# Optimization experiments

Hardware: AMD Instinct MI355X
Metric: run time of the kernel (lower is better)

Reference implementation:

```python
import jax, jax.numpy as jnp
import numpy as np

N_MICS = 8
MIC_RADIUS = 0.05
SAMPLE_RATE = 16000.0
SPEED_SOUND = 343.0
EPS = 1e-20
SPHERE_LEVELS = 4


def sphere_np(levels=SPHERE_LEVELS):
    # Faithful numpy port of the torch icosphere subdivision in sphere().
    h = 5.0 ** 0.5 / 5.0
    r = 2.0 / 5.0 * 5.0 ** 0.5
    pi = 3.141592654
    pts = np.zeros((12, 3), dtype=np.float32)
    pts[0] = [0.0, 0.0, 1.0]
    pts[11] = [0.0, 0.0, -1.0]
    k = np.arange(5, dtype=np.float32)
    pts[1:6, 0] = r * np.sin(2.0 * pi * k / 5.0)
    pts[1:6, 1] = r * np.cos(2.0 * pi * k / 5.0)
    pts[1:6, 2] = h
    pts[6:11, 0] = -r * np.sin(2.0 * pi * k / 5.0)
    pts[6:11, 1] = -r * np.cos(2.0 * pi * k / 5.0)
    pts[6:11, 2] = -h
    trs = np.array([[0, 2, 1], [0, 3, 2], [0, 4, 3], [0, 5, 4], [0, 1, 5],
                    [9, 1, 2], [10, 2, 3], [6, 3, 4], [7, 4, 5], [8, 5, 1],
                    [4, 7, 6], [5, 8, 7], [1, 9, 8], [2, 10, 9], [3, 6, 10],
                    [11, 6, 7], [11, 7, 8], [11, 8, 9], [11, 9, 10], [11, 10, 6]], dtype=np.int64)
    for _ in range(levels):
        T = trs.shape[0]
        sub = np.zeros((4 * T, 6), dtype=np.int64)
        sub[0 * T:1 * T] = trs[:, [0, 0, 0, 1, 2, 0]]
        sub[1 * T:2 * T] = trs[:, [0, 1, 1, 1, 1, 2]]
        sub[2 * T:3 * T] = trs[:, [2, 0, 1, 2, 2, 2]]
        sub[3 * T:4 * T] = trs[:, [0, 1, 1, 2, 2, 0]]
        flat = np.concatenate((sub[:, [0, 1]], sub[:, [2, 3]], sub[:, [4, 5]]), axis=0)
        srt = np.sort(flat, axis=1)
        m = srt.max()
        scal = srt[:, 0] * (m + 1) + srt[:, 1]
        uniq, inv = np.unique(scal, return_inverse=True)
        uv0 = uniq // (m + 1)
        uv1 = uniq - uv0 * (m + 1)
        trs = inv.reshape(3, -1).T
        pts = pts[uv0] + pts[uv1]
        pts /= np.sqrt((pts ** 2).sum(axis=1, keepdims=True))
    return pts.astype(np.float32)


def setup_inputs() -> dict:
    key = jax.random.key(0)
    # DOA grid and TDOAs from array geometry (precomputed in SrpPhat.__init__)
    doas_np = sphere_np()                                    # [2562, 3]
    ang = 2.0 * np.pi * np.arange(N_MICS) / N_MICS
    mics_np = np.stack([MIC_RADIUS * np.cos(ang), MIC_RADIUS * np.sin(ang),
                        np.zeros(N_MICS)], axis=1).astype(np.float32)  # [8, 3]
    taus_np = (SAMPLE_RATE / SPEED_SOUND) * (doas_np @ mics_np.T)      # [2562, 8]
    B, T, F, P = 4, 250, 513, N_MICS * (N_MICS + 1) // 2
    XXs = jax.random.normal(key, (B, T, F, 2, P), dtype=jnp.float32)
    return {"XXs": XXs, "taus": jnp.asarray(taus_np), "doas": jnp.asarray(doas_np)}


def reference(XXs, taus, doas):
    B, T, F, _, P = XXs.shape
    n_mics = taus.shape[1]
    D = taus.shape[0]
    frame_size = (F - 1) * 2
    # Steering phases: a = exp(-j * omega * tau)   [D, F, M]
    omegas = 2.0 * jnp.pi * jnp.arange(F, dtype=jnp.float32) / frame_size
    phase = omegas[None, :, None] * taus[:, None, :]
    A_re = jnp.cos(phase)
    A_im = -jnp.sin(phase)
    # Cross steering terms for every mic pair (triu incl. diagonal): W = a_i * conj(a_j)^H form
    i0, i1 = np.triu_indices(n_mics)                         # 36 pairs for 8 mics
    Ws_re = A_re[:, :, i0] * A_re[:, :, i1] + A_im[:, :, i0] * A_im[:, :, i1]  # [D, F, P]
    Ws_im = A_re[:, :, i0] * A_im[:, :, i1] - A_im[:, :, i0] * A_re[:, :, i1]
    # PHAT normalization of the cross-spectra
    XX_re = XXs[:, :, :, 0, :]
    XX_im = XXs[:, :, :, 1, :]
    mag = jnp.sqrt(XX_re ** 2 + XX_im ** 2) + EPS
    Xr = (XX_re / mag).reshape(B, T, F * P)
    Xi = (XX_im / mag).reshape(B, T, F * P)
    Wr = Ws_re.reshape(D, F * P)
    Wi = Ws_im.reshape(D, F * P)
    # SRP map: Re{ sum_fp XX_norm * conj(W) } reduced over freqs and pairs
    Ys = jnp.matmul(Xr, Wr.T) + jnp.matmul(Xi, Wi.T)         # [B, T, D]
    idx = jnp.argmax(Ys, axis=2)                             # [B, T]
    return doas[idx]                                         # [B, T, 3]
```

## Files before the change

kernel.cpp:

```cpp
#include <hip/hip_runtime.h>
#include <math.h>


#define F_BINS  513
#define M_TOTAL 1000
#define D_TOTAL 2562
#define D_PAD   2688
#define NPAIR   28
#define NC      32
#define K2      (NPAIR * NC)
#define S_SCALE 4.67f
#define NBT     4
#define CNT     8
#define FSPLIT  12
#define KSPB    4
#define KPS     224
#define BT_PAD  1024

#define OFF_COEF 0
#define OFF_TT   16512
#define OFF_GT   (OFF_TT + (size_t)K2 * D_PAD)
#define OFF_GP   (OFF_GT + (size_t)K2 * BT_PAD)
#define OFF_YS   OFF_GP

__device__ __constant__ int c_ptab[NPAIR] = {1,2,3,4,5,6,7, 9,10,11,12,13,14,
                                             16,17,18,19,20, 22,23,24,25,
                                             27,28,29, 31,32, 34};
__device__ __constant__ int c_i0[NPAIR] = {0,0,0,0,0,0,0, 1,1,1,1,1,1,
                                           2,2,2,2,2, 3,3,3,3, 4,4,4, 5,5, 6};
__device__ __constant__ int c_i1[NPAIR] = {1,2,3,4,5,6,7, 2,3,4,5,6,7,
                                           3,4,5,6,7, 4,5,6,7, 5,6,7, 6,7, 7};
__device__ __constant__ int c_inv[36] = {
    -1, 0, 1, 2, 3, 4, 5, 6,
    -1, 7, 8, 9,10,11,12,
    -1,13,14,15,16,17,
    -1,18,19,20,21,
    -1,22,23,24,
    -1,25,26,
    -1,27,
    -1};

__global__ void k_coef(float* __restrict__ coefEO) {
    __shared__ double sHC[NC][NC + 1];
    __shared__ double sHS[NC][NC + 1];
    const int f = blockIdx.x;
    const int t = threadIdx.x;
    const double z = (double)f * (M_PI / 512.0) * (double)S_SCALE;
    double th = M_PI * (t + 0.5) / NC;
    double ct = cos(th);
    double hs, hc;
    sincos(z * ct, &hs, &hc);
    double cp = 1.0, cc = ct, c2 = 2.0 * ct;
    sHC[0][t] = hc;      sHS[0][t] = hs;
    sHC[1][t] = hc * cc; sHS[1][t] = hs * cc;
    for (int n = 2; n < NC; ++n) {
        double cn = c2 * cc - cp;
        cp = cc; cc = cn;
        sHC[n][t] = hc * cn;
        sHS[n][t] = hs * cn;
    }
    __syncthreads();
    const int n = (t < 16) ? 2 * t : 2 * (t - 16) + 1;
    double sum = 0.0;
    if (t < 16) { for (int j = 0; j < NC; ++j) sum += sHC[n][j]; }
    else        { for (int j = 0; j < NC; ++j) sum += sHS[n][j]; }
    double scale = (n == 0) ? (1.0 / NC) : (2.0 / NC);
    coefEO[f * 32 + t] = (float)(sum * scale);
}

__global__ void k_ttab(const float* __restrict__ taus, float* __restrict__ Tt) {
    const int d = blockIdx.x * 256 + threadIdx.x;
    const int p = blockIdx.y;
    if (d >= D_PAD) return;
    const bool live = d < D_TOTAL;
    const int dd = live ? d : 0;
    const float u = (taus[dd * 8 + c_i0[p]] - taus[dd * 8 + c_i1[p]]) * (1.0f / S_SCALE);
    float* base = Tt + (size_t)p * 32 * D_PAD + d;
    base[0] = live ? 1.f : 0.f;
    base[(size_t)16 * D_PAD] = live ? u : 0.f;
    float tp = 1.f, tc = u;
    const float u2 = 2.f * u;
    for (int n = 2; n < NC; ++n) {
        float tn = u2 * tc - tp;
        tp = tc; tc = tn;
        int c = (n & 1) ? 16 + (n >> 1) : (n >> 1);
        base[(size_t)c * D_PAD] = live ? tn : 0.f;
    }
}

#define NSLOT 3
__global__ __launch_bounds__(128, 3) void k_stageA(
    const float* __restrict__ XXs, const float* __restrict__ coefEO,
    float* __restrict__ Gp)
{
    __shared__ float4 sXn4[NBT][CNT / 4][64];
    __shared__ float  sCall[48][32];
    const int t     = threadIdx.x;
    const int bt0   = blockIdx.x * NBT;
    const int split = blockIdx.y;
    const int fbeg  = (F_BINS * split) / FSPLIT;
    const int fend  = (F_BINS * (split + 1)) / FSPLIT;
    const int p   = t & 31;
    const int sel = t >> 5;
    const bool im = sel >= 2;
    const int row = (p < NPAIR ? p : NPAIR - 1) + (im ? 32 : 0);
    const int c0  = (sel & 1) * 8 + (im ? 16 : 0);

    for (int e = t; e < 48 * 8; e += 128) {
        int fl = e >> 3, q = e & 7;
        int f  = fbeg + fl; if (f > F_BINS - 1) f = F_BINS - 1;
        *(float4*)&sCall[fl][q * 4] = *(const float4*)&coefEO[f * 32 + q * 4];
    }

    const float* srcs[NSLOT];
    float*       dstb[NSLOT];
    int          offj[NSLOT][4];
    int          flv [NSLOT];
    #pragma unroll
    for (int s = 0; s < NSLOT; ++s) {
        int e    = t + s * 128;
        bool act = e < NBT * CNT * 9;
        int ec  = act ? e : 0;
        int q   = ec % 9;
        int rbf = ec / 9;
        int bt  = rbf / CNT;
        int fl  = rbf - bt * CNT;
        flv[s]  = act ? fl : 127;
        srcs[s] = XXs + (((size_t)(bt0 + bt) * F_BINS) + fl) * 72 + q * 4;
        dstb[s] = (float*)&sXn4[bt][fl >> 2][0] + (fl & 3);
        #pragma unroll
        for (int j = 0; j < 4; ++j) {
            int pp = c_inv[q * 4 + j];
            offj[s][j] = (act && pp >= 0) ? pp * 4 : -1;
        }
    }

    float acc[NBT][8] = {};
    float4 cur_re[NSLOT], cur_im[NSLOT], nxt_re[NSLOT], nxt_im[NSLOT];

    auto issue = [&](int fc, float4* vre, float4* vim) {
        const int cnt = fend - fc;
        #pragma unroll
        for (int s = 0; s < NSLOT; ++s) {
            float4 z4 = {0.f, 0.f, 0.f, 0.f};
            vre[s] = z4; vim[s] = z4;
            if (flv[s] < cnt) {
                const float* bp = srcs[s] + (size_t)fc * 72;
                vre[s] = *(const float4*)bp;
                vim[s] = *(const float4*)(bp + 36);
            }
        }
    };

    issue(fbeg, cur_re, cur_im);

    for (int fc = fbeg; fc < fend; fc += CNT) {
        __syncthreads();
        #pragma unroll
        for (int s = 0; s < NSLOT; ++s) {
            const float* xr4 = (const float*)&cur_re[s];
            const float* xi4 = (const float*)&cur_im[s];
            #pragma unroll
            for (int j = 0; j < 4; ++j) {
                int o = offj[s][j];
                if (o >= 0) {
                    float xr = xr4[j], xi = xi4[j];
                    float inv = rsqrtf(xr * xr + xi * xi + 1e-37f);
                    dstb[s][o]       = xr * inv;
                    dstb[s][o + 128] = xi * inv;
                }
            }
        }
        if (fc + CNT < fend) issue(fc + CNT, nxt_re, nxt_im);
        __syncthreads();
        const int cbase = fc - fbeg;
        #pragma unroll
        for (int fg = 0; fg < CNT / 4; ++fg) {
            float4 cjA[4], cjB[4];
            #pragma unroll
            for (int j = 0; j < 4; ++j) {
                cjA[j] = *(const float4*)&sCall[cbase + fg * 4 + j][c0];
                cjB[j] = *(const float4*)&sCall[cbase + fg * 4 + j][c0 + 4];
            }
            #pragma unroll
            for (int bt = 0; bt < NBT; ++bt) {
                float4 a4 = sXn4[bt][fg][row];
                float av[4] = {a4.x, a4.y, a4.z, a4.w};
                #pragma unroll
                for (int j = 0; j < 4; ++j) {
                    acc[bt][0] = fmaf(av[j], cjA[j].x, acc[bt][0]);
                    acc[bt][1] = fmaf(av[j], cjA[j].y, acc[bt][1]);
                    acc[bt][2] = fmaf(av[j], cjA[j].z, acc[bt][2]);
                    acc[bt][3] = fmaf(av[j], cjA[j].w, acc[bt][3]);
                    acc[bt][4] = fmaf(av[j], cjB[j].x, acc[bt][4]);
                    acc[bt][5] = fmaf(av[j], cjB[j].y, acc[bt][5]);
                    acc[bt][6] = fmaf(av[j], cjB[j].z, acc[bt][6]);
                    acc[bt][7] = fmaf(av[j], cjB[j].w, acc[bt][7]);
                }
            }
        }
        #pragma unroll
        for (int s = 0; s < NSLOT; ++s) { cur_re[s] = nxt_re[s]; cur_im[s] = nxt_im[s]; }
    }

    if (p < NPAIR) {
        float* gsp = Gp + (size_t)split * M_TOTAL * K2;
        #pragma unroll
        for (int bt = 0; bt < NBT; ++bt) {
            float* g = gsp + (size_t)(bt0 + bt) * K2 + p * 32 + c0;
            float4 v0 = {acc[bt][0], acc[bt][1], acc[bt][2], acc[bt][3]};
            float4 v1 = {acc[bt][4], acc[bt][5], acc[bt][6], acc[bt][7]};
            *(float4*)&g[0] = v0;
            *(float4*)&g[4] = v1;
        }
    }
}

__global__ __launch_bounds__(256) void k_reduceG(
    const float* __restrict__ Gp, float* __restrict__ Gt)
{
    __shared__ float sT[32][65];
    const int t   = threadIdx.x;
    const int k0  = blockIdx.x * 32;
    const int bt0 = blockIdx.y * 64;
    const size_t MK = (size_t)M_TOTAL * K2;
    #pragma unroll
    for (int i = 0; i < 8; ++i) {
        int e  = t + i * 256;
        int kl = e & 31, btl = e >> 5;
        int bt = bt0 + btl;
        float s = 0.f;
        if (bt < M_TOTAL) {
            const float* g = Gp + (size_t)bt * K2 + k0 + kl;
            #pragma unroll
            for (int pl = 0; pl < FSPLIT; ++pl) s += g[pl * MK];
        }
        sT[kl][btl] = s;
    }
    __syncthreads();
    #pragma unroll
    for (int i = 0; i < 8; ++i) {
        int e   = t + i * 256;
        int btl = e & 63, kl = e >> 6;
        Gt[(size_t)(k0 + kl) * BT_PAD + bt0 + btl] = sT[kl][btl];
    }
}

#define BKB 32
__global__ __launch_bounds__(256, 4) void k_gemmB(
    const float* __restrict__ Gt, const float* __restrict__ Tt,
    float* __restrict__ Ysp)
{
    __shared__ float sA[BKB][260];
    __shared__ float sB[BKB][68];
    const int t = threadIdx.x;
    const int row0 = blockIdx.x * 256;
    const int col0 = blockIdx.y * 64;
    const int koff = blockIdx.z * KPS;
    const int tx = t & 15;
    const int ty = t >> 4;
    float acc[16][4] = {};

    for (int k0 = 0; k0 < KPS; k0 += BKB) {
        __syncthreads();
        #pragma unroll
        for (int i = 0; i < 8; ++i) {
            int e = t + i * 256;
            int kk = e >> 6, r4 = (e & 63) * 4;
            *(float4*)&sA[kk][r4] =
                *(const float4*)&Gt[(size_t)(koff + k0 + kk) * BT_PAD + row0 + r4];
        }
        #pragma unroll
        for (int i = 0; i < 2; ++i) {
            int e = t + i * 256;
            int kk = e >> 4, c4 = (e & 15) * 4;
            *(float4*)&sB[kk][c4] =
                *(const float4*)&Tt[(size_t)(koff + k0 + kk) * D_PAD + col0 + c4];
        }
        __syncthreads();
        #pragma unroll 8
        for (int kk = 0; kk < BKB; ++kk) {
            float4 b  = *(const float4*)&sB[kk][tx * 4];
            float4 a0 = *(const float4*)&sA[kk][ty * 16];
            float4 a1 = *(const float4*)&sA[kk][ty * 16 + 4];
            float4 a2 = *(const float4*)&sA[kk][ty * 16 + 8];
            float4 a3 = *(const float4*)&sA[kk][ty * 16 + 12];
            float av[16] = {a0.x, a0.y, a0.z, a0.w, a1.x, a1.y, a1.z, a1.w,
                            a2.x, a2.y, a2.z, a2.w, a3.x, a3.y, a3.z, a3.w};
            float bv[4] = {b.x, b.y, b.z, b.w};
            #pragma unroll
            for (int i = 0; i < 16; ++i)
                #pragma unroll
                for (int j = 0; j < 4; ++j)
                    acc[i][j] = fmaf(av[i], bv[j], acc[i][j]);
        }
    }
    float* yp = Ysp + (size_t)blockIdx.z * M_TOTAL * D_PAD;
    #pragma unroll
    for (int i = 0; i < 16; ++i) {
        int rg = row0 + ty * 16 + i;
        if (rg >= M_TOTAL) continue;
        float4 v = {acc[i][0], acc[i][1], acc[i][2], acc[i][3]};
        *(float4*)(yp + (size_t)rg * D_PAD + col0 + tx * 4) = v;
    }
}

__global__ __launch_bounds__(256) void k_argmax(
    const float* __restrict__ Ysp, const float* __restrict__ doas,
    float* __restrict__ out)
{
    __shared__ float sv[256];
    __shared__ int   si[256];
    const int row = blockIdx.x;
    const int tid = threadIdx.x;
    const float* y = Ysp + (size_t)row * D_PAD;
    const size_t PL = (size_t)M_TOTAL * D_PAD;
    float best = -INFINITY;
    int bi = D_TOTAL;
    for (int d = tid; d < D_TOTAL; d += 256) {
        float v = y[d] + y[d + PL] + y[d + 2 * PL] + y[d + 3 * PL];
        if (v > best) { best = v; bi = d; }
    }
    sv[tid] = best; si[tid] = bi;
    __syncthreads();
    for (int s = 128; s > 0; s >>= 1) {
        if (tid < s) {
            float v2 = sv[tid + s]; int i2 = si[tid + s];
            if (v2 > sv[tid] || (v2 == sv[tid] && i2 < si[tid])) { sv[tid] = v2; si[tid] = i2; }
        }
        __syncthreads();
    }
    if (tid == 0) {
        int idx = si[0];
        out[row * 3 + 0] = doas[idx * 3 + 0];
        out[row * 3 + 1] = doas[idx * 3 + 1];
        out[row * 3 + 2] = doas[idx * 3 + 2];
    }
}

extern "C" void kernel_launch(void* const* d_in, const int* in_sizes, int n_in,
                              void* d_out, int out_size, void* d_ws, size_t ws_size,
                              hipStream_t stream) {
    const float* XXs  = (const float*)d_in[0];
    const float* taus = (const float*)d_in[1];
    const float* doas = (const float*)d_in[2];
    float* ws     = (float*)d_ws;
    float* coefEO = ws + OFF_COEF;
    float* Tt     = ws + OFF_TT;
    float* Gt     = ws + OFF_GT;
    float* Gp     = ws + OFF_GP;
    float* Ysp    = ws + OFF_YS;

    k_coef   <<<F_BINS, 32, 0, stream>>>(coefEO);
    k_ttab   <<<dim3((D_PAD + 255) / 256, NPAIR), 256, 0, stream>>>(taus, Tt);
    k_stageA <<<dim3(M_TOTAL / NBT, FSPLIT), 128, 0, stream>>>(XXs, coefEO, Gp);
    k_reduceG<<<dim3(K2 / 32, BT_PAD / 64), 256, 0, stream>>>(Gp, Gt);
    k_gemmB  <<<dim3(BT_PAD / 256, D_PAD / 64, KSPB), 256, 0, stream>>>(Gt, Tt, Ysp);
    k_argmax <<<M_TOTAL, 256, 0, stream>>>(Ysp, doas, (float*)d_out);
}
```

Measured before the change: 319.9 us.

## Double-buffer stageA shared tiles and merge coef/ttab init kernels

The stage-A loop now keeps two shared-memory buffers for the normalized cross-spectra and alternates between two register sets. This drops one barrier per chunk and lets the normalize of the next chunk overlap with compute on the current one. The two setup kernels that build the Chebyshev coefficients and the steering table are fused into a single launch, chosen by block index, which saves one kernel launch. In exchange it uses more LDS and registers in stageA, which could lower occupancy, and the coefficient blocks now launch 256 threads of which only 32 do work.

```diff
diff --git a/kernel.cpp b/kernel.cpp
--- a/kernel.cpp
+++ b/kernel.cpp
@@ -16,6 +16,7 @@
 #define KSPB    4
 #define KPS     224
 #define BT_PAD  1024
+#define DBLK    11
 
 #define OFF_COEF 0
 #define OFF_TT   16512
@@ -23,9 +24,6 @@
 #define OFF_GP   (OFF_GT + (size_t)K2 * BT_PAD)
 #define OFF_YS   OFF_GP
 
-__device__ __constant__ int c_ptab[NPAIR] = {1,2,3,4,5,6,7, 9,10,11,12,13,14,
-                                             16,17,18,19,20, 22,23,24,25,
-                                             27,28,29, 31,32, 34};
 __device__ __constant__ int c_i0[NPAIR] = {0,0,0,0,0,0,0, 1,1,1,1,1,1,
                                            2,2,2,2,2, 3,3,3,3, 4,4,4, 5,5, 6};
 __device__ __constant__ int c_i1[NPAIR] = {1,2,3,4,5,6,7, 2,3,4,5,6,7,
@@ -40,51 +38,56 @@
     -1,27,
     -1};
 
-__global__ void k_coef(float* __restrict__ coefEO) {
+__global__ void k_init(const float* __restrict__ taus,
+                       float* __restrict__ coefEO, float* __restrict__ Tt) {
     __shared__ double sHC[NC][NC + 1];
     __shared__ double sHS[NC][NC + 1];
-    const int f = blockIdx.x;
-    const int t = threadIdx.x;
-    const double z = (double)f * (M_PI / 512.0) * (double)S_SCALE;
-    double th = M_PI * (t + 0.5) / NC;
-    double ct = cos(th);
-    double hs, hc;
-    sincos(z * ct, &hs, &hc);
-    double cp = 1.0, cc = ct, c2 = 2.0 * ct;
-    sHC[0][t] = hc;      sHS[0][t] = hs;
-    sHC[1][t] = hc * cc; sHS[1][t] = hs * cc;
-    for (int n = 2; n < NC; ++n) {
-        double cn = c2 * cc - cp;
-        cp = cc; cc = cn;
-        sHC[n][t] = hc * cn;
-        sHS[n][t] = hs * cn;
-    }
-    __syncthreads();
-    const int n = (t < 16) ? 2 * t : 2 * (t - 16) + 1;
-    double sum = 0.0;
-    if (t < 16) { for (int j = 0; j < NC; ++j) sum += sHC[n][j]; }
-    else        { for (int j = 0; j < NC; ++j) sum += sHS[n][j]; }
-    double scale = (n == 0) ? (1.0 / NC) : (2.0 / NC);
-    coefEO[f * 32 + t] = (float)(sum * scale);
-}
-
-__global__ void k_ttab(const float* __restrict__ taus, float* __restrict__ Tt) {
-    const int d = blockIdx.x * 256 + threadIdx.x;
-    const int p = blockIdx.y;
-    if (d >= D_PAD) return;
-    const bool live = d < D_TOTAL;
-    const int dd = live ? d : 0;
-    const float u = (taus[dd * 8 + c_i0[p]] - taus[dd * 8 + c_i1[p]]) * (1.0f / S_SCALE);
-    float* base = Tt + (size_t)p * 32 * D_PAD + d;
-    base[0] = live ? 1.f : 0.f;
-    base[(size_t)16 * D_PAD] = live ? u : 0.f;
-    float tp = 1.f, tc = u;
-    const float u2 = 2.f * u;
-    for (int n = 2; n < NC; ++n) {
-        float tn = u2 * tc - tp;
-        tp = tc; tc = tn;
-        int c = (n & 1) ? 16 + (n >> 1) : (n >> 1);
-        base[(size_t)c * D_PAD] = live ? tn : 0.f;
+    if (blockIdx.x < DBLK * NPAIR) {
+        const int p = blockIdx.x / DBLK;
+        const int d = (blockIdx.x % DBLK) * 256 + threadIdx.x;
+        if (d >= D_PAD) return;
+        const bool live = d < D_TOTAL;
+        const int dd = live ? d : 0;
+        const float u = (taus[dd * 8 + c_i0[p]] - taus[dd * 8 + c_i1[p]]) * (1.0f / S_SCALE);
+        float* base = Tt + (size_t)p * 32 * D_PAD + d;
+        base[0] = live ? 1.f : 0.f;
+        base[(size_t)16 * D_PAD] = live ? u : 0.f;
+        float tp = 1.f, tc = u;
+        const float u2 = 2.f * u;
+        for (int n = 2; n < NC; ++n) {
+            float tn = u2 * tc - tp;
+            tp = tc; tc = tn;
+            int c = (n & 1) ? 16 + (n >> 1) : (n >> 1);
+            base[(size_t)c * D_PAD] = live ? tn : 0.f;
+        }
+    } else {
+        const int f = blockIdx.x - DBLK * NPAIR;
+        const int t = threadIdx.x;
+        if (t < 32) {
+            const double z = (double)f * (M_PI / 512.0) * (double)S_SCALE;
+            double th = M_PI * (t + 0.5) / NC;
+            double ct = cos(th);
+            double hs, hc;
+            sincos(z * ct, &hs, &hc);
+            double cp = 1.0, cc = ct, c2 = 2.0 * ct;
+            sHC[0][t] = hc;      sHS[0][t] = hs;
+            sHC[1][t] = hc * cc; sHS[1][t] = hs * cc;
+            for (int n = 2; n < NC; ++n) {
+                double cn = c2 * cc - cp;
+                cp = cc; cc = cn;
+                sHC[n][t] = hc * cn;
+                sHS[n][t] = hs * cn;
+            }
+        }
+        __syncthreads();
+        if (t < 32) {
+            const int n = (t < 16) ? 2 * t : 2 * (t - 16) + 1;
+            double sum = 0.0;
+            if (t < 16) { for (int j = 0; j < NC; ++j) sum += sHC[n][j]; }
+            else        { for (int j = 0; j < NC; ++j) sum += sHS[n][j]; }
+            double scale = (n == 0) ? (1.0 / NC) : (2.0 / NC);
+            coefEO[f * 32 + t] = (float)(sum * scale);
+        }
     }
 }
 
@@ -93,7 +96,7 @@
     const float* __restrict__ XXs, const float* __restrict__ coefEO,
     float* __restrict__ Gp)
 {
-    __shared__ float4 sXn4[NBT][CNT / 4][64];
+    __shared__ float4 sXn4[2][NBT][CNT / 4][64];
     __shared__ float  sCall[48][32];
     const int t     = threadIdx.x;
     const int bt0   = blockIdx.x * NBT;
@@ -127,7 +130,7 @@
         int fl  = rbf - bt * CNT;
         flv[s]  = act ? fl : 127;
         srcs[s] = XXs + (((size_t)(bt0 + bt) * F_BINS) + fl) * 72 + q * 4;
-        dstb[s] = (float*)&sXn4[bt][fl >> 2][0] + (fl & 3);
+        dstb[s] = (float*)&sXn4[0][bt][fl >> 2][0] + (fl & 3);
         #pragma unroll
         for (int j = 0; j < 4; ++j) {
             int pp = c_inv[q * 4 + j];
@@ -136,9 +139,9 @@
     }
 
     float acc[NBT][8] = {};
-    float4 cur_re[NSLOT], cur_im[NSLOT], nxt_re[NSLOT], nxt_im[NSLOT];
-
-    auto issue = [&](int fc, float4* vre, float4* vim) {
+    float4 Are[NSLOT], Aim[NSLOT], Bre[NSLOT], Bim[NSLOT];
+
+    auto issue = [&](int fc, float4 (&vre)[NSLOT], float4 (&vim)[NSLOT]) {
         const int cnt = fend - fc;
         #pragma unroll
         for (int s = 0; s < NSLOT; ++s) {
@@ -152,27 +155,27 @@
         }
     };
 
-    issue(fbeg, cur_re, cur_im);
-
-    for (int fc = fbeg; fc < fend; fc += CNT) {
-        __syncthreads();
+    auto normalize = [&](float4 (&cre)[NSLOT], float4 (&cim)[NSLOT], int b) {
+        const int boff = b * (NBT * (CNT / 4) * 64 * 4);
         #pragma unroll
         for (int s = 0; s < NSLOT; ++s) {
-            const float* xr4 = (const float*)&cur_re[s];
-            const float* xi4 = (const float*)&cur_im[s];
+            const float* xr4 = (const float*)&cre[s];
+            const float* xi4 = (const float*)&cim[s];
+            float* dst = dstb[s] + boff;
             #pragma unroll
             for (int j = 0; j < 4; ++j) {
                 int o = offj[s][j];
                 if (o >= 0) {
                     float xr = xr4[j], xi = xi4[j];
                     float inv = rsqrtf(xr * xr + xi * xi + 1e-37f);
-                    dstb[s][o]       = xr * inv;
-                    dstb[s][o + 128] = xi * inv;
+                    dst[o]       = xr * inv;
+                    dst[o + 128] = xi * inv;
                 }
             }
         }
-        if (fc + CNT < fend) issue(fc + CNT, nxt_re, nxt_im);
-        __syncthreads();
+    };
+
+    auto compute = [&](int fc, int b) {
         const int cbase = fc - fbeg;
         #pragma unroll
         for (int fg = 0; fg < CNT / 4; ++fg) {
@@ -184,7 +187,7 @@
             }
             #pragma unroll
             for (int bt = 0; bt < NBT; ++bt) {
-                float4 a4 = sXn4[bt][fg][row];
+                float4 a4 = sXn4[b][bt][fg][row];
                 float av[4] = {a4.x, a4.y, a4.z, a4.w};
                 #pragma unroll
                 for (int j = 0; j < 4; ++j) {
@@ -199,8 +202,23 @@
                 }
             }
         }
-        #pragma unroll
-        for (int s = 0; s < NSLOT; ++s) { cur_re[s] = nxt_re[s]; cur_im[s] = nxt_im[s]; }
+    };
+
+    issue(fbeg, Are, Aim);
+    int b = 0;
+    for (int fc = fbeg; fc < fend; fc += 2 * CNT) {
+        if (fc + CNT < fend) issue(fc + CNT, Bre, Bim);
+        normalize(Are, Aim, b);
+        __syncthreads();
+        compute(fc, b);
+        b ^= 1;
+        if (fc + CNT < fend) {
+            if (fc + 2 * CNT < fend) issue(fc + 2 * CNT, Are, Aim);
+            normalize(Bre, Bim, b);
+            __syncthreads();
+            compute(fc + CNT, b);
+            b ^= 1;
+        }
     }
 
     if (p < NPAIR) {
@@ -351,8 +369,7 @@
     float* Gp     = ws + OFF_GP;
     float* Ysp    = ws + OFF_YS;
 
-    k_coef   <<<F_BINS, 32, 0, stream>>>(coefEO);
-    k_ttab   <<<dim3((D_PAD + 255) / 256, NPAIR), 256, 0, stream>>>(taus, Tt);
+    k_init   <<<DBLK * NPAIR + F_BINS, 256, 0, stream>>>(taus, coefEO, Tt);
     k_stageA <<<dim3(M_TOTAL / NBT, FSPLIT), 128, 0, stream>>>(XXs, coefEO, Gp);
     k_reduceG<<<dim3(K2 / 32, BT_PAD / 64), 256, 0, stream>>>(Gp, Gt);
     k_gemmB  <<<dim3(BT_PAD / 256, D_PAD / 64, KSPB), 256, 0, stream>>>(Gt, Tt, Ysp);
```

After: 408.0 us. +27.6%, slower.
